# Performance work log

Measured on AMD Instinct MI355X. Metric: run time of the kernel, lower is better.

Reference implementation:

```python
import jax, jax.numpy as jnp
import numpy as np

B = 2_000_000
OVERLAP_WEIGHT = 0.5
EPS = 1e-6


def setup_inputs() -> dict:
    key = jax.random.key(0)
    k1, k2 = jax.random.split(key)
    preds = jax.random.normal(k1, (B, 10), dtype=jnp.float32)
    targets = jax.random.normal(k2, (B, 10), dtype=jnp.float32)
    return {"preds": preds, "targets": targets}


def _quat_to_rot(q):
    # q: (B,4) in xyzw order, assumed normalized. Returns (B,3,3),
    # matching the (transposed-convention) matrix in the torch source.
    x, y, z, w = q[:, 0], q[:, 1], q[:, 2], q[:, 3]
    r = jnp.stack([
        1 - 2 * y * y - 2 * z * z, 2 * x * y + 2 * z * w, 2 * x * z - 2 * y * w,
        2 * x * y - 2 * z * w, 1 - 2 * x * x - 2 * z * z, 2 * y * z + 2 * x * w,
        2 * x * z + 2 * y * w, 2 * y * z - 2 * x * w, 1 - 2 * x * x - 2 * y * y,
    ], axis=-1)
    return r.reshape(-1, 3, 3)


def _overlaps(pred_params, gt_params):
    pred_c, pred_d, pred_q = pred_params[:, :3], pred_params[:, 3:6], pred_params[:, 6:]
    gt_c, gt_d, gt_q = gt_params[:, :3], gt_params[:, 3:6], gt_params[:, 6:]
    pred_q = pred_q / jnp.linalg.norm(pred_q, axis=-1, keepdims=True)
    gt_q = gt_q / jnp.linalg.norm(gt_q, axis=-1, keepdims=True)
    pred_rot = _quat_to_rot(pred_q)  # (B,3,3)
    gt_rot = _quat_to_rot(gt_q)      # (B,3,3)
    # trace(pred_rot.T @ gt_rot) = sum of elementwise products
    rot_align = jnp.clip(jnp.sum(pred_rot * gt_rot, axis=(1, 2)) / 3.0, 0.0, 1.0)
    pred_ext = jnp.abs(jnp.einsum('bij,bj->bi', pred_rot, pred_d / 2))
    gt_ext = jnp.abs(jnp.einsum('bij,bj->bi', gt_rot, gt_d / 2))
    center_diff = jnp.abs(pred_c - gt_c)
    overlap_per_axis = jnp.maximum(jnp.minimum(pred_ext, gt_ext) * 2 - center_diff, 0.0) \
        / (pred_ext + gt_ext + EPS)
    overlap = jnp.prod(overlap_per_axis, axis=-1) * rot_align
    return jnp.clip(overlap, 0.0, 1.0)


def _smooth_l1(preds, targets):
    d = preds - targets
    ad = jnp.abs(d)
    return jnp.mean(jnp.where(ad < 1.0, 0.5 * d * d, ad - 0.5))


def reference(preds, targets):
    param_loss = _smooth_l1(preds, targets)
    overlap = _overlaps(preds, targets)
    return param_loss + OVERLAP_WEIGHT * (1.0 - jnp.mean(overlap))
```

## Files before the change

kernel.cpp:

```cpp
#include <hip/hip_runtime.h>


#define B_ROWS 2000000
#define THREADS 512
#define CHUNK_ROWS 512
#define CHUNK_F4 1280
#define N_CHUNKS 3907
constexpr float OVERLAP_WEIGHT = 0.5f;
constexpr float EPS_F = 1e-6f;
constexpr size_t TOTAL_F4 = (size_t)B_ROWS * 40 / 16;

__device__ __forceinline__ void gload_lds16(const float* g, float* l) {
    __builtin_amdgcn_global_load_lds(
        (const __attribute__((address_space(1))) void*)g,
        (__attribute__((address_space(3))) void*)l, 16, 0, 0);
}

__device__ __forceinline__ void quat_to_rot(float x, float y, float z, float w,
                                            float R[9]) {
    R[0] = 1.f - 2.f*y*y - 2.f*z*z;
    R[1] = 2.f*x*y + 2.f*z*w;
    R[2] = 2.f*x*z - 2.f*y*w;
    R[3] = 2.f*x*y - 2.f*z*w;
    R[4] = 1.f - 2.f*x*x - 2.f*z*z;
    R[5] = 2.f*y*z + 2.f*x*w;
    R[6] = 2.f*x*z + 2.f*y*w;
    R[7] = 2.f*y*z - 2.f*x*w;
    R[8] = 1.f - 2.f*x*x - 2.f*y*y;
}

__global__ __launch_bounds__(THREADS) void hybrid_loss_main(
    const float* __restrict__ preds, const float* __restrict__ targets,
    float* __restrict__ acc)
{
    __shared__ __align__(16) float ldsP[CHUNK_F4 * 4];
    __shared__ __align__(16) float ldsT[CHUNK_F4 * 4];

    const int tid  = threadIdx.x;
    const int wave = tid >> 6;
    const int lane = tid & 63;
    const int c    = blockIdx.x;
    const size_t base_f4 = (size_t)c * CHUNK_F4;

    #pragma unroll
    for (int r = 0; r < 2; ++r) {
        const int e_wave = r * 512 + wave * 64;
        size_t gidx = base_f4 + e_wave + lane;
        if (gidx >= TOTAL_F4) gidx = TOTAL_F4 - 1;
        gload_lds16(preds   + gidx * 4, &ldsP[e_wave * 4]);
        gload_lds16(targets + gidx * 4, &ldsT[e_wave * 4]);
    }
    if (wave < 4) {
        const int e_wave = 1024 + wave * 64;
        size_t gidx = base_f4 + e_wave + lane;
        if (gidx >= TOTAL_F4) gidx = TOTAL_F4 - 1;
        gload_lds16(preds   + gidx * 4, &ldsP[e_wave * 4]);
        gload_lds16(targets + gidx * 4, &ldsT[e_wave * 4]);
    }
    __syncthreads();

    float psum = 0.f, osum = 0.f;
    const size_t grow = (size_t)c * CHUNK_ROWS + tid;
    if (grow < B_ROWS) {
        float p[10], t[10];
        const float2* lp = reinterpret_cast<const float2*>(&ldsP[tid * 10]);
        const float2* lt = reinterpret_cast<const float2*>(&ldsT[tid * 10]);
        #pragma unroll
        for (int i = 0; i < 5; ++i) {
            float2 a = lp[i]; p[2*i] = a.x; p[2*i+1] = a.y;
            float2 b = lt[i]; t[2*i] = b.x; t[2*i+1] = b.y;
        }

        #pragma unroll
        for (int i = 0; i < 10; ++i) {
            float d  = p[i] - t[i];
            float ad = fabsf(d);
            psum += (ad < 1.f) ? 0.5f * d * d : ad - 0.5f;
        }

        float pqn = sqrtf(p[6]*p[6] + p[7]*p[7] + p[8]*p[8] + p[9]*p[9]);
        float tqn = sqrtf(t[6]*t[6] + t[7]*t[7] + t[8]*t[8] + t[9]*t[9]);
        float pri = 1.f / pqn, tri = 1.f / tqn;
        float PR[9], TR[9];
        quat_to_rot(p[6]*pri, p[7]*pri, p[8]*pri, p[9]*pri, PR);
        quat_to_rot(t[6]*tri, t[7]*tri, t[8]*tri, t[9]*tri, TR);

        float ra = 0.f;
        #pragma unroll
        for (int i = 0; i < 9; ++i) ra += PR[i] * TR[i];
        ra = fminf(fmaxf(ra * (1.f/3.f), 0.f), 1.f);

        float ov = ra;
        #pragma unroll
        for (int i = 0; i < 3; ++i) {
            float pe = fabsf(PR[3*i+0]*(p[3]*0.5f) + PR[3*i+1]*(p[4]*0.5f) + PR[3*i+2]*(p[5]*0.5f));
            float te = fabsf(TR[3*i+0]*(t[3]*0.5f) + TR[3*i+1]*(t[4]*0.5f) + TR[3*i+2]*(t[5]*0.5f));
            float cd = fabsf(p[i] - t[i]);
            float ax = fmaxf(fminf(pe, te) * 2.f - cd, 0.f) / (pe + te + EPS_F);
            ov *= ax;
        }
        ov = fminf(fmaxf(ov, 0.f), 1.f);
        osum += ov;
    }

    #pragma unroll
    for (int off = 32; off > 0; off >>= 1) {
        psum += __shfl_down(psum, off);
        osum += __shfl_down(osum, off);
    }
    __syncthreads();
    if (lane == 0) { ldsP[wave] = psum; ldsP[8 + wave] = osum; }
    __syncthreads();
    if (tid == 0) {
        float P = 0.f, O = 0.f;
        #pragma unroll
        for (int w = 0; w < 8; ++w) { P += ldsP[w]; O += ldsP[8 + w]; }
        atomicAdd(&acc[0], P);
        atomicAdd(&acc[1], O);
    }
}

__global__ void hybrid_loss_finalize(const float* __restrict__ acc,
                                     float* __restrict__ out) {
    out[0] = acc[0] * (1.f / (10.f * (float)B_ROWS))
           + OVERLAP_WEIGHT * (1.f - acc[1] * (1.f / (float)B_ROWS));
}

extern "C" void kernel_launch(void* const* d_in, const int* in_sizes, int n_in,
                              void* d_out, int out_size, void* d_ws, size_t ws_size,
                              hipStream_t stream) {
    const float* preds   = (const float*)d_in[0];
    const float* targets = (const float*)d_in[1];
    float* out = (float*)d_out;
    float* acc = (float*)d_ws;

    hipMemsetAsync(acc, 0, 2 * sizeof(float), stream);

    hybrid_loss_main<<<N_CHUNKS, THREADS, 0, stream>>>(preds, targets, acc);
    hybrid_loss_finalize<<<1, 1, 0, stream>>>(acc, out);
}
```

Measured before the change: 231.8 us.

## Use persistent blocks with register-prefetched chunks staged through LDS

Replaces the one-block-per-chunk launch with a 1024-block persistent grid of 256 threads that loops over chunks. Each iteration loads the next chunk's float4s into registers while computing the current chunk from LDS, so global loads overlap compute. The direct global-to-LDS loads are dropped in favor of register loads followed by LDS stores. Per-block launch and reduction overhead and atomic traffic go down, at the cost of lower occupancy per block and two barriers per chunk.

```diff
diff --git a/kernel.cpp b/kernel.cpp
--- a/kernel.cpp
+++ b/kernel.cpp
@@ -2,19 +2,14 @@
 
 
 #define B_ROWS 2000000
-#define THREADS 512
+#define THREADS 256
 #define CHUNK_ROWS 512
 #define CHUNK_F4 1280
 #define N_CHUNKS 3907
+#define GRID 1024
 constexpr float OVERLAP_WEIGHT = 0.5f;
 constexpr float EPS_F = 1e-6f;
-constexpr size_t TOTAL_F4 = (size_t)B_ROWS * 40 / 16;
-
-__device__ __forceinline__ void gload_lds16(const float* g, float* l) {
-    __builtin_amdgcn_global_load_lds(
-        (const __attribute__((address_space(1))) void*)g,
-        (__attribute__((address_space(3))) void*)l, 16, 0, 0);
-}
+constexpr int TOTAL_F4 = 5000000;
 
 __device__ __forceinline__ void quat_to_rot(float x, float y, float z, float w,
                                             float R[9]) {
@@ -30,77 +25,104 @@
 }
 
 __global__ __launch_bounds__(THREADS) void hybrid_loss_main(
-    const float* __restrict__ preds, const float* __restrict__ targets,
+    const float4* __restrict__ preds4, const float4* __restrict__ targets4,
     float* __restrict__ acc)
 {
-    __shared__ __align__(16) float ldsP[CHUNK_F4 * 4];
-    __shared__ __align__(16) float ldsT[CHUNK_F4 * 4];
+    __shared__ __align__(16) float4 ldsP[CHUNK_F4];
+    __shared__ __align__(16) float4 ldsT[CHUNK_F4];
 
     const int tid  = threadIdx.x;
     const int wave = tid >> 6;
     const int lane = tid & 63;
-    const int c    = blockIdx.x;
-    const size_t base_f4 = (size_t)c * CHUNK_F4;
+    const int spos = wave * 320 + lane;
 
-    #pragma unroll
-    for (int r = 0; r < 2; ++r) {
-        const int e_wave = r * 512 + wave * 64;
-        size_t gidx = base_f4 + e_wave + lane;
-        if (gidx >= TOTAL_F4) gidx = TOTAL_F4 - 1;
-        gload_lds16(preds   + gidx * 4, &ldsP[e_wave * 4]);
-        gload_lds16(targets + gidx * 4, &ldsT[e_wave * 4]);
-    }
-    if (wave < 4) {
-        const int e_wave = 1024 + wave * 64;
-        size_t gidx = base_f4 + e_wave + lane;
-        if (gidx >= TOTAL_F4) gidx = TOTAL_F4 - 1;
-        gload_lds16(preds   + gidx * 4, &ldsP[e_wave * 4]);
-        gload_lds16(targets + gidx * 4, &ldsT[e_wave * 4]);
-    }
-    __syncthreads();
+    float4 rp[5], rt[5];
+    float psum = 0.f, osum = 0.f;
 
-    float psum = 0.f, osum = 0.f;
-    const size_t grow = (size_t)c * CHUNK_ROWS + tid;
-    if (grow < B_ROWS) {
-        float p[10], t[10];
-        const float2* lp = reinterpret_cast<const float2*>(&ldsP[tid * 10]);
-        const float2* lt = reinterpret_cast<const float2*>(&ldsT[tid * 10]);
+    int c = blockIdx.x;
+    {
+        const int gb = c * CHUNK_F4;
         #pragma unroll
         for (int i = 0; i < 5; ++i) {
-            float2 a = lp[i]; p[2*i] = a.x; p[2*i+1] = a.y;
-            float2 b = lt[i]; t[2*i] = b.x; t[2*i+1] = b.y;
+            int idx = gb + spos + i * 64;
+            if (idx >= TOTAL_F4) idx = TOTAL_F4 - 1;
+            rp[i] = preds4[idx];
+            rt[i] = targets4[idx];
+        }
+    }
+
+    while (true) {
+        #pragma unroll
+        for (int i = 0; i < 5; ++i) {
+            ldsP[spos + i * 64] = rp[i];
+            ldsT[spos + i * 64] = rt[i];
+        }
+        __syncthreads();
+
+        const int cn = c + GRID;
+        const bool more = (cn < N_CHUNKS);
+        if (more) {
+            const int gb = cn * CHUNK_F4;
+            #pragma unroll
+            for (int i = 0; i < 5; ++i) {
+                int idx = gb + spos + i * 64;
+                if (idx >= TOTAL_F4) idx = TOTAL_F4 - 1;
+                rp[i] = preds4[idx];
+                rt[i] = targets4[idx];
+            }
         }
 
+        const int rowbase = c * CHUNK_ROWS;
         #pragma unroll
-        for (int i = 0; i < 10; ++i) {
-            float d  = p[i] - t[i];
-            float ad = fabsf(d);
-            psum += (ad < 1.f) ? 0.5f * d * d : ad - 0.5f;
+        for (int k = 0; k < 2; ++k) {
+            const int rr = tid + k * 256;
+            if (rowbase + rr < B_ROWS) {
+                float p[10], t[10];
+                const float2* lp = reinterpret_cast<const float2*>(
+                    reinterpret_cast<const float*>(ldsP) + rr * 10);
+                const float2* lt = reinterpret_cast<const float2*>(
+                    reinterpret_cast<const float*>(ldsT) + rr * 10);
+                #pragma unroll
+                for (int i = 0; i < 5; ++i) {
+                    float2 a = lp[i]; p[2*i] = a.x; p[2*i+1] = a.y;
+                    float2 b = lt[i]; t[2*i] = b.x; t[2*i+1] = b.y;
+                }
+
+                #pragma unroll
+                for (int i = 0; i < 10; ++i) {
+                    float d  = p[i] - t[i];
+                    float ad = fabsf(d);
+                    psum += (ad < 1.f) ? 0.5f * d * d : ad - 0.5f;
+                }
+
+                float pqn = sqrtf(p[6]*p[6] + p[7]*p[7] + p[8]*p[8] + p[9]*p[9]);
+                float tqn = sqrtf(t[6]*t[6] + t[7]*t[7] + t[8]*t[8] + t[9]*t[9]);
+                float pri = 1.f / pqn, tri = 1.f / tqn;
+                float PR[9], TR[9];
+                quat_to_rot(p[6]*pri, p[7]*pri, p[8]*pri, p[9]*pri, PR);
+                quat_to_rot(t[6]*tri, t[7]*tri, t[8]*tri, t[9]*tri, TR);
+
+                float ra = 0.f;
+                #pragma unroll
+                for (int i = 0; i < 9; ++i) ra += PR[i] * TR[i];
+                ra = fminf(fmaxf(ra * (1.f/3.f), 0.f), 1.f);
+
+                float ov = ra;
+                #pragma unroll
+                for (int i = 0; i < 3; ++i) {
+                    float pe = fabsf(PR[3*i+0]*(p[3]*0.5f) + PR[3*i+1]*(p[4]*0.5f) + PR[3*i+2]*(p[5]*0.5f));
+                    float te = fabsf(TR[3*i+0]*(t[3]*0.5f) + TR[3*i+1]*(t[4]*0.5f) + TR[3*i+2]*(t[5]*0.5f));
+                    float cd = fabsf(p[i] - t[i]);
+                    float ax = fmaxf(fminf(pe, te) * 2.f - cd, 0.f) / (pe + te + EPS_F);
+                    ov *= ax;
+                }
+                ov = fminf(fmaxf(ov, 0.f), 1.f);
+                osum += ov;
+            }
         }
-
-        float pqn = sqrtf(p[6]*p[6] + p[7]*p[7] + p[8]*p[8] + p[9]*p[9]);
-        float tqn = sqrtf(t[6]*t[6] + t[7]*t[7] + t[8]*t[8] + t[9]*t[9]);
-        float pri = 1.f / pqn, tri = 1.f / tqn;
-        float PR[9], TR[9];
-        quat_to_rot(p[6]*pri, p[7]*pri, p[8]*pri, p[9]*pri, PR);
-        quat_to_rot(t[6]*tri, t[7]*tri, t[8]*tri, t[9]*tri, TR);
-
-        float ra = 0.f;
-        #pragma unroll
-        for (int i = 0; i < 9; ++i) ra += PR[i] * TR[i];
-        ra = fminf(fmaxf(ra * (1.f/3.f), 0.f), 1.f);
-
-        float ov = ra;
-        #pragma unroll
-        for (int i = 0; i < 3; ++i) {
-            float pe = fabsf(PR[3*i+0]*(p[3]*0.5f) + PR[3*i+1]*(p[4]*0.5f) + PR[3*i+2]*(p[5]*0.5f));
-            float te = fabsf(TR[3*i+0]*(t[3]*0.5f) + TR[3*i+1]*(t[4]*0.5f) + TR[3*i+2]*(t[5]*0.5f));
-            float cd = fabsf(p[i] - t[i]);
-            float ax = fmaxf(fminf(pe, te) * 2.f - cd, 0.f) / (pe + te + EPS_F);
-            ov *= ax;
-        }
-        ov = fminf(fmaxf(ov, 0.f), 1.f);
-        osum += ov;
+        __syncthreads();
+        if (!more) break;
+        c = cn;
     }
 
     #pragma unroll
@@ -108,13 +130,12 @@
         psum += __shfl_down(psum, off);
         osum += __shfl_down(osum, off);
     }
-    __syncthreads();
-    if (lane == 0) { ldsP[wave] = psum; ldsP[8 + wave] = osum; }
+    float* red = reinterpret_cast<float*>(ldsP);
+    if (lane == 0) { red[wave] = psum; red[4 + wave] = osum; }
     __syncthreads();
     if (tid == 0) {
-        float P = 0.f, O = 0.f;
-        #pragma unroll
-        for (int w = 0; w < 8; ++w) { P += ldsP[w]; O += ldsP[8 + w]; }
+        float P = red[0] + red[1] + red[2] + red[3];
+        float O = red[4] + red[5] + red[6] + red[7];
         atomicAdd(&acc[0], P);
         atomicAdd(&acc[1], O);
     }
@@ -129,13 +150,13 @@
 extern "C" void kernel_launch(void* const* d_in, const int* in_sizes, int n_in,
                               void* d_out, int out_size, void* d_ws, size_t ws_size,
                               hipStream_t stream) {
-    const float* preds   = (const float*)d_in[0];
-    const float* targets = (const float*)d_in[1];
+    const float4* preds4   = (const float4*)d_in[0];
+    const float4* targets4 = (const float4*)d_in[1];
     float* out = (float*)d_out;
     float* acc = (float*)d_ws;
 
     hipMemsetAsync(acc, 0, 2 * sizeof(float), stream);
 
-    hybrid_loss_main<<<N_CHUNKS, THREADS, 0, stream>>>(preds, targets, acc);
+    hybrid_loss_main<<<GRID, THREADS, 0, stream>>>(preds4, targets4, acc);
     hybrid_loss_finalize<<<1, 1, 0, stream>>>(acc, out);
 }
```

New measurement: 210.9 us. -9.0%, faster.
